# Kernel optimization log

Hardware: AMD Instinct MI355X
Metric: run time of the kernel (lower is better)

Reference implementation:

```python
import jax, jax.numpy as jnp
import numpy as np

B, A, Bdim, C = 8, 256, 256, 64  # batch, height a, width b, channels
F = Bdim // 2 + 1                 # rfft width


def setup_inputs() -> dict:
    key = jax.random.key(0)
    k1, k2, k3 = jax.random.split(key, 3)
    x = jax.random.normal(k1, (B, A, Bdim, C), dtype=jnp.float32)
    # complex spectral weight stored as two float planes, shape [a, f, C]
    scale = 1.0 / (A * Bdim)
    w_real = jax.random.normal(k2, (A, F, C), dtype=jnp.float32) * scale
    w_imag = jax.random.normal(k3, (A, F, C), dtype=jnp.float32) * scale
    return {"x": x, "w_real": w_real, "w_imag": w_imag}


def reference(x, w_real, w_imag):
    # Depthwise FNO-style spectral conv:
    #   y[b,:,:,c] = irfft2( rfft2(x[b,:,:,c]) * W[:,:,c] )
    # The CUDA version packs BHWC -> planar [B*C,a,b], runs cuFFT R2C,
    # multiplies by W [a,f,C] elementwise in the spectrum, C2R, and scales
    # by 1/(a*b) (cuFFT is unnormalized). jnp.fft.irfft2 already applies
    # the 1/(a*b) normalization, so layouts/scale fold away here.
    a, b = x.shape[1], x.shape[2]
    W = jax.lax.complex(w_real, w_imag)          # [a, f, C] complex64
    Xf = jnp.fft.rfft2(x, axes=(1, 2))           # [B, a, f, C]
    y = jnp.fft.irfft2(Xf * W[None], s=(a, b), axes=(1, 2))
    return y.astype(x.dtype)
```

## Files before the change

kernel.cpp:

```cpp
#include <hip/hip_runtime.h>
#include <math.h>

#define NB 8
#define NA 256
#define NBD 256
#define NC 64
#define NF 129

struct alignas(8) cpx { float re, im; };

__device__ __forceinline__ cpx cmul(cpx a, cpx b){
  cpx r;
  r.re = fmaf(a.re, b.re, -(a.im * b.im));
  r.im = fmaf(a.re, b.im,  a.im * b.re);
  return r;
}

__device__ __forceinline__ int PHY(int n, int g){
  return (n << 5) | ((g + n + (n >> 4)) & 31);
}

__global__ void k0_twiddle(float2* __restrict__ tw){
  int k = threadIdx.x;
  double ang = 6.283185307179586476925286766559 * (double)k / 256.0;
  tw[k] = make_float2((float)cos(ang), (float)sin(ang));
}

template<int SIGN>
__device__ __forceinline__ void fft16(cpx a[16]){
  cpx tmp;
  #define SW(i,j) tmp = a[i]; a[i] = a[j]; a[j] = tmp;
  SW(1,8) SW(2,4) SW(3,12) SW(5,10) SW(7,14) SW(11,13)
  #undef SW
  const float CT[8] = {1.f, 0.92387953251128674f, 0.70710678118654752f, 0.38268343236508977f,
                       0.f, -0.38268343236508977f, -0.70710678118654752f, -0.92387953251128674f};
  const float ST[8] = {0.f, 0.38268343236508977f, 0.70710678118654752f, 0.92387953251128674f,
                       1.f, 0.92387953251128674f, 0.70710678118654752f, 0.38268343236508977f};
  #pragma unroll
  for (int s = 1; s <= 4; ++s){
    const int m = 1 << s, half = m >> 1, str = 16 >> s;
    #pragma unroll
    for (int k = 0; k < 16; k += m){
      #pragma unroll
      for (int j = 0; j < half; ++j){
        cpx w; w.re = CT[j*str]; w.im = (float)SIGN * ST[j*str];
        cpx t = cmul(a[k+j+half], w);
        cpx u = a[k+j];
        a[k+j].re      = u.re + t.re; a[k+j].im      = u.im + t.im;
        a[k+j+half].re = u.re - t.re; a[k+j+half].im = u.im - t.im;
      }
    }
  }
}

template<int SIGN>
__device__ __forceinline__ void fft256_col(cpx* __restrict__ tile, int g, int t,
                                           const float2* __restrict__ tw){
  cpx a[16];
  #pragma unroll
  for (int n1 = 0; n1 < 16; ++n1) a[n1] = tile[PHY(16*n1 + t, g)];
  fft16<SIGN>(a);
  #pragma unroll
  for (int k1 = 1; k1 < 16; ++k1){
    float2 tv = tw[(t * k1) & 255];
    cpx w; w.re = tv.x; w.im = (SIGN < 0) ? -tv.y : tv.y;
    a[k1] = cmul(a[k1], w);
  }
  #pragma unroll
  for (int k1 = 0; k1 < 16; ++k1) tile[PHY(16*k1 + t, g)] = a[k1];
  __syncthreads();

  cpx b[16];
  #pragma unroll
  for (int n2 = 0; n2 < 16; ++n2) b[n2] = tile[PHY(16*t + n2, g)];
  fft16<SIGN>(b);
  __syncthreads();
  #pragma unroll
  for (int k2 = 0; k2 < 16; ++k2) tile[PHY(t + 16*k2, g)] = b[k2];
  __syncthreads();
}

__global__ __launch_bounds__(512) void k1_rfft_b(const float* __restrict__ x,
                                                 float4* __restrict__ mid4,
                                                 const float2* __restrict__ tw){
  __shared__ cpx tile[256*32];
  const int tid = threadIdx.x;
  const int blk = blockIdx.x;
  const int bb = blk >> 8, a = blk & 255;
  const int g = tid >> 4, t = tid & 15;

  const float4* src = (const float4*)(x + (size_t)blk * (NBD * NC));
  #pragma unroll
  for (int it = 0; it < 8; ++it){
    int idx = it*512 + tid;
    int j = idx >> 4, q = idx & 15;
    float4 v = src[idx];
    cpx p0; p0.re = v.x; p0.im = v.y;
    cpx p1; p1.re = v.z; p1.im = v.w;
    tile[PHY(j, 2*q)]   = p0;
    tile[PHY(j, 2*q+1)] = p1;
  }
  __syncthreads();

  fft256_col<-1>(tile, g, t, tw);

  for (int it = 0; it < 9; ++it){
    int idx = it*512 + tid;
    if (idx < NF*32){
      int k = idx >> 5, gg = idx & 31;
      cpx zk = tile[PHY(k, gg)];
      cpx zm = tile[PHY((256 - k) & 255, gg)];
      float4 o;
      o.x = 0.5f*(zk.re + zm.re);
      o.y = 0.5f*(zk.im - zm.im);
      o.z = 0.5f*(zk.im + zm.im);
      o.w = 0.5f*(zm.re - zk.re);
      mid4[(((size_t)bb*NF + k)*256 + a)*32 + gg] = o;
    }
  }
}

__global__ __launch_bounds__(512) void k2_fft_a_mul(float2* __restrict__ mid2,
                                                    const float* __restrict__ wre,
                                                    const float* __restrict__ wim,
                                                    const float2* __restrict__ tw){
  __shared__ cpx tile[256*32];
  const int tid = threadIdx.x;
  int blk = blockIdx.x;
  const int h = blk & 1; blk >>= 1;
  const int f = blk % NF, bb = blk / NF;
  const int g = tid >> 4, t = tid & 15;
  const int c0 = h * 32;

  float2* base = mid2 + ((size_t)bb*NF + f) * (256*64) + c0;
  #pragma unroll
  for (int it = 0; it < 16; ++it){
    int idx = it*512 + tid;
    int a = idx >> 5, gc = idx & 31;
    float2 v = base[(size_t)a*64 + gc];
    cpx z; z.re = v.x; z.im = v.y;
    tile[PHY(a, gc)] = z;
  }
  __syncthreads();

  fft256_col<-1>(tile, g, t, tw);

  #pragma unroll
  for (int it = 0; it < 16; ++it){
    int idx = it*512 + tid;
    int ka = idx >> 5, gc = idx & 31;
    size_t wi = ((size_t)ka*NF + f)*64 + (c0 + gc);
    cpx w; w.re = wre[wi] * (1.0f/65536.0f); w.im = wim[wi] * (1.0f/65536.0f);
    cpx v = tile[PHY(ka, gc)];
    tile[PHY(ka, gc)] = cmul(v, w);
  }
  __syncthreads();

  fft256_col<+1>(tile, g, t, tw);

  #pragma unroll
  for (int it = 0; it < 16; ++it){
    int idx = it*512 + tid;
    int a = idx >> 5, gc = idx & 31;
    cpx v = tile[PHY(a, gc)];
    float2 o; o.x = v.re; o.y = v.im;
    base[(size_t)a*64 + gc] = o;
  }
}

__global__ __launch_bounds__(512) void k3_irfft_b(const float4* __restrict__ mid4,
                                                  float2* __restrict__ y2,
                                                  const float2* __restrict__ tw){
  __shared__ cpx tile[256*32];
  const int tid = threadIdx.x;
  const int blk = blockIdx.x;
  const int bb = blk >> 8, a = blk & 255;
  const int g = tid >> 4, t = tid & 15;

  for (int it = 0; it < 9; ++it){
    int idx = it*512 + tid;
    if (idx < NF*32){
      int f = idx >> 5, gg = idx & 31;
      float4 v = mid4[(((size_t)bb*NF + f)*256 + a)*32 + gg];
      cpx sd;
      if (f == 0 || f == 128){
        sd.re = v.x;
        sd.im = v.z;
      } else {
        sd.re = v.x - v.w; sd.im = v.y + v.z;
      }
      tile[PHY(f, gg)] = sd;
      if (f >= 1 && f <= 127){
        cpx se; se.re = v.x + v.w; se.im = v.z - v.y;
        tile[PHY(256 - f, gg)] = se;
      }
    }
  }
  __syncthreads();

  fft256_col<+1>(tile, g, t, tw);

  float2* dst = y2 + (size_t)blk * (256*32);
  #pragma unroll
  for (int it = 0; it < 16; ++it){
    int idx = it*512 + tid;
    int n = idx >> 5, gg = idx & 31;
    cpx v = tile[PHY(n, gg)];
    float2 o; o.x = v.re; o.y = v.im;
    dst[(size_t)n*32 + gg] = o;
  }
}

extern "C" void kernel_launch(void* const* d_in, const int* in_sizes, int n_in,
                              void* d_out, int out_size, void* d_ws, size_t ws_size,
                              hipStream_t stream){
  const float* x   = (const float*)d_in[0];
  const float* wre = (const float*)d_in[1];
  const float* wim = (const float*)d_in[2];

  float2* tw = (float2*)d_ws;
  float*  mid = (float*)d_ws + 512;

  k0_twiddle  <<<1,   256, 0, stream>>>(tw);
  k1_rfft_b   <<<NB*NA,    512, 0, stream>>>(x, (float4*)mid, tw);
  k2_fft_a_mul<<<NB*NF*2,  512, 0, stream>>>((float2*)mid, wre, wim, tw);
  k3_irfft_b  <<<NB*NA,    512, 0, stream>>>((const float4*)mid, (float2*)d_out, tw);
}
```

Baseline: 203.4 us.

## Fuse forward and inverse column FFTs around spectral multiply in registers

In the column-FFT kernel, the forward second radix-16 stage, the weight multiply and the inverse first radix-16 stage now run on the same register array, with no shared-memory round trips in between. The weights are loaded directly into registers, and the loads are issued before the FFT work. This cuts several LDS passes and barriers. A launch-bounds hint of 4 blocks per CU is also added, which may limit registers and risk spills given the larger live state.

```diff
diff --git a/kernel.cpp b/kernel.cpp
--- a/kernel.cpp
+++ b/kernel.cpp
@@ -120,10 +120,10 @@
   }
 }
 
-__global__ __launch_bounds__(512) void k2_fft_a_mul(float2* __restrict__ mid2,
-                                                    const float* __restrict__ wre,
-                                                    const float* __restrict__ wim,
-                                                    const float2* __restrict__ tw){
+__global__ __launch_bounds__(512, 4) void k2_fft_a_mul(float2* __restrict__ mid2,
+                                                       const float* __restrict__ wre,
+                                                       const float* __restrict__ wim,
+                                                       const float2* __restrict__ tw){
   __shared__ cpx tile[256*32];
   const int tid = threadIdx.x;
   int blk = blockIdx.x;
@@ -143,20 +143,63 @@
   }
   __syncthreads();
 
-  fft256_col<-1>(tile, g, t, tw);
-
-  #pragma unroll
-  for (int it = 0; it < 16; ++it){
-    int idx = it*512 + tid;
-    int ka = idx >> 5, gc = idx & 31;
-    size_t wi = ((size_t)ka*NF + f)*64 + (c0 + gc);
-    cpx w; w.re = wre[wi] * (1.0f/65536.0f); w.im = wim[wi] * (1.0f/65536.0f);
-    cpx v = tile[PHY(ka, gc)];
-    tile[PHY(ka, gc)] = cmul(v, w);
-  }
-  __syncthreads();
-
-  fft256_col<+1>(tile, g, t, tw);
+  {
+    cpx a[16];
+    #pragma unroll
+    for (int n1 = 0; n1 < 16; ++n1) a[n1] = tile[PHY(16*n1 + t, g)];
+    fft16<-1>(a);
+    #pragma unroll
+    for (int k1 = 1; k1 < 16; ++k1){
+      float2 tv = tw[(t * k1) & 255];
+      cpx w; w.re = tv.x; w.im = -tv.y;
+      a[k1] = cmul(a[k1], w);
+    }
+    #pragma unroll
+    for (int k1 = 0; k1 < 16; ++k1) tile[PHY(16*k1 + t, g)] = a[k1];
+  }
+  __syncthreads();
+
+  float wr[16], wi_[16];
+  #pragma unroll
+  for (int k2 = 0; k2 < 16; ++k2){
+    size_t wi = ((size_t)(t + 16*k2)*NF + f)*64 + (c0 + g);
+    wr[k2]  = wre[wi];
+    wi_[k2] = wim[wi];
+  }
+
+  cpx b[16];
+  #pragma unroll
+  for (int n2 = 0; n2 < 16; ++n2) b[n2] = tile[PHY(16*t + n2, g)];
+  fft16<-1>(b);
+
+  #pragma unroll
+  for (int k2 = 0; k2 < 16; ++k2){
+    cpx w; w.re = wr[k2] * (1.0f/65536.0f); w.im = wi_[k2] * (1.0f/65536.0f);
+    b[k2] = cmul(b[k2], w);
+  }
+
+  fft16<1>(b);
+  #pragma unroll
+  for (int k1 = 1; k1 < 16; ++k1){
+    float2 tv = tw[(t * k1) & 255];
+    cpx w; w.re = tv.x; w.im = tv.y;
+    b[k1] = cmul(b[k1], w);
+  }
+  __syncthreads();
+  #pragma unroll
+  for (int k1 = 0; k1 < 16; ++k1) tile[PHY(16*k1 + t, g)] = b[k1];
+  __syncthreads();
+
+  {
+    cpx c[16];
+    #pragma unroll
+    for (int n2 = 0; n2 < 16; ++n2) c[n2] = tile[PHY(16*t + n2, g)];
+    fft16<1>(c);
+    __syncthreads();
+    #pragma unroll
+    for (int k2 = 0; k2 < 16; ++k2) tile[PHY(t + 16*k2, g)] = c[k2];
+  }
+  __syncthreads();
 
   #pragma unroll
   for (int it = 0; it < 16; ++it){
```

Measured after the change: 258.5 us. 1.27x slower.
